# Kernel optimization log

Hardware: AMD Instinct MI355X
Metric: run time of the kernel (lower is better)

## Reference

```python
import jax, jax.numpy as jnp
import numpy as np

EPS = 1e-6
HEAD_DIM = 64
N_Q = 16
N_KV = 2

def setup_inputs() -> dict:
    key = jax.random.key(0)
    ks = jax.random.split(key, 4)
    H = 1024
    x = jax.random.normal(ks[0], (4, 8192, H), dtype=jnp.float32)
    ln_weight = jnp.zeros((H,), dtype=jnp.float32)  # Gemma param; scale is (1 + w)
    wq = jax.random.normal(ks[1], (H, HEAD_DIM * N_Q), dtype=jnp.float32) / np.sqrt(H)
    wk = jax.random.normal(ks[2], (H, HEAD_DIM * N_KV), dtype=jnp.float32) / np.sqrt(H)
    wv = jax.random.normal(ks[3], (H, HEAD_DIM * N_KV), dtype=jnp.float32) / np.sqrt(H)
    return {"x": x, "ln_weight": ln_weight, "wq": wq, "wk": wk, "wv": wv}

def gemma_rms_norm(x, w):
    xf = x.astype(jnp.float32)
    h = xf * jax.lax.rsqrt(jnp.mean(xf * xf, axis=-1, keepdims=True) + EPS)
    return (h * (1.0 + w.astype(jnp.float32))).astype(x.dtype)

def reference(x, ln_weight, wq, wk, wv):
    # Gemma RMSNorm prologue, then three linear projections (no bias).
    h = gemma_rms_norm(x, ln_weight)            # [B, S, H]
    q = jnp.einsum('bsh,hd->bsd', h, wq)        # [B, S, nq*d]
    k = jnp.einsum('bsh,hd->bsd', h, wk)        # [B, S, nkv*d]
    v = jnp.einsum('bsh,hd->bsd', h, wv)
    B, S = x.shape[0], x.shape[1]
    q = q.reshape(B, S, N_Q, HEAD_DIM)
    k = k.reshape(B, S, N_KV, HEAD_DIM)
    v = v.reshape(B, S, N_KV, HEAD_DIM)
    return (q, k, v)
```

## Files before the change

kernel.cpp:

```cpp
#include <hip/hip_runtime.h>
#include <hip/hip_bf16.h>

typedef __attribute__((ext_vector_type(4))) float f32x4;
typedef __attribute__((ext_vector_type(8))) short bf16x8;

#define H 1024
#define NTOT 1280
#define BM 256
#define BN 256
#define BK 64
#define NKT (H / BK)

static __device__ __forceinline__ unsigned short f2bf(float f) {
    __hip_bfloat16 b = __float2bfloat16(f);
    return __builtin_bit_cast(unsigned short, b);
}

#define GLOAD_LDS16(g, l)                                                     \
    __builtin_amdgcn_global_load_lds(                                         \
        (const __attribute__((address_space(1))) void*)(g),                   \
        (__attribute__((address_space(3))) void*)(l), 16, 0, 0)

__global__ __launch_bounds__(256) void k_rms(const float* __restrict__ x,
                                             __hip_bfloat16* __restrict__ h) {
    const int wave = threadIdx.x >> 6;
    const int lane = threadIdx.x & 63;
    const size_t row = (size_t)blockIdx.x * 4 + wave;

    const float4* xr = (const float4*)(x + row * H);
    float4 v[4];
    float ss = 0.f;
#pragma unroll
    for (int i = 0; i < 4; ++i) {
        v[i] = xr[lane + 64 * i];
        ss += v[i].x * v[i].x + v[i].y * v[i].y + v[i].z * v[i].z + v[i].w * v[i].w;
    }
#pragma unroll
    for (int o = 1; o < 64; o <<= 1) ss += __shfl_xor(ss, o);
    const float sc = rsqrtf(ss * (1.0f / H) + 1e-6f);

    ushort4* hr = (ushort4*)(h + row * H);
#pragma unroll
    for (int i = 0; i < 4; ++i) {
        ushort4 o4;
        o4.x = f2bf(v[i].x * sc);
        o4.y = f2bf(v[i].y * sc);
        o4.z = f2bf(v[i].z * sc);
        o4.w = f2bf(v[i].w * sc);
        hr[lane + 64 * i] = o4;
    }
}

__global__ __launch_bounds__(256) void k_wprep(const float* __restrict__ wq,
                                               const float* __restrict__ wk,
                                               const float* __restrict__ wv,
                                               const float* __restrict__ lnw,
                                               __hip_bfloat16* __restrict__ Bt) {
    const int idx = blockIdx.x * 256 + threadIdx.x;
    const int n = idx >> 10;
    const int k = idx & 1023;
    const float s = 1.0f + lnw[k];
    float w;
    if (n < 1024)       w = wq[k * 1024 + n];
    else if (n < 1152)  w = wk[k * 128 + (n - 1024)];
    else                w = wv[k * 128 + (n - 1152)];
    Bt[idx] = __float2bfloat16(s * w);
}

__global__ __launch_bounds__(512, 2) void k_gemm(const __hip_bfloat16* __restrict__ A,
                                                 const __hip_bfloat16* __restrict__ Bt,
                                                 float* __restrict__ out, int rows) {
    __shared__ __align__(16) char smem[131072];

    const int tid = threadIdx.x;
    const int lane = tid & 63;
    const int wid = tid >> 6;
    const int wm = wid >> 2;
    const int wn = wid & 3;

    const int nwg = gridDim.x;
    const int q8 = nwg >> 3, r8 = nwg & 7;
    const int xcd = blockIdx.x & 7, rank = blockIdx.x >> 3;
    const int wg = (xcd < r8 ? xcd * (q8 + 1) : r8 * (q8 + 1) + (xcd - r8) * q8) + rank;
    const int nt = wg % (NTOT / BN);
    const int mt = wg / (NTOT / BN);
    const size_t m0 = (size_t)mt * BM;

    const int cswz = ((tid & 7) * 16) ^ (((tid >> 3) & 7) << 4);
    const char* aG = (const char*)A + (m0 + (tid >> 3)) * (size_t)(H * 2) + cswz;
    const char* bG = (const char*)Bt + ((size_t)nt * BN + (tid >> 3)) * (size_t)(H * 2) + cswz;

#define STAGE(buf, kt)                                                        \
    {                                                                         \
        const char* as_ = aG + (size_t)(kt) * (BK * 2);                       \
        const char* bs_ = bG + (size_t)(kt) * (BK * 2);                       \
        char* ld_ = smem + (buf) * 65536 + tid * 16;                          \
        _Pragma("unroll") for (int j = 0; j < 4; ++j)                         \
            GLOAD_LDS16(as_ + (size_t)j * 64 * (H * 2), ld_ + j * 8192);      \
        _Pragma("unroll") for (int j = 0; j < 4; ++j)                         \
            GLOAD_LDS16(bs_ + (size_t)j * 64 * (H * 2), ld_ + 32768 + j * 8192); \
    }

    const int rowA = wm * 128 + (lane & 15);
    const int rowB = wn * 64 + (lane & 15);
    const int xm = (lane & 7) << 4;
    const int c0 = (((lane >> 4) * 16)) ^ xm;
    const int c1 = (64 + ((lane >> 4) * 16)) ^ xm;

    f32x4 acc[8][4] = {};

    STAGE(0, 0);
    STAGE(1, 1);

#define ITER(kt, DOSTAGE, VMSTR)                                              \
    {                                                                         \
        const int cur_ = (kt) & 1;                                            \
        const char* aLb = smem + cur_ * 65536;                                \
        const char* bLb = aLb + 32768;                                        \
        asm volatile("s_waitcnt vmcnt(" VMSTR ")" ::: "memory");              \
        __builtin_amdgcn_s_barrier();                                         \
        __builtin_amdgcn_sched_barrier(0);                                    \
        bf16x8 a0[8], b0[4];                                                  \
        _Pragma("unroll") for (int mi = 0; mi < 8; ++mi)                      \
            a0[mi] = *(const bf16x8*)(aLb + (rowA + mi * 16) * 128 + c0);     \
        _Pragma("unroll") for (int ni = 0; ni < 4; ++ni)                      \
            b0[ni] = *(const bf16x8*)(bLb + (rowB + ni * 16) * 128 + c0);     \
        _Pragma("unroll") for (int mi = 0; mi < 8; ++mi)                      \
            _Pragma("unroll") for (int ni = 0; ni < 4; ++ni)                  \
                acc[mi][ni] = __builtin_amdgcn_mfma_f32_16x16x32_bf16(        \
                    a0[mi], b0[ni], acc[mi][ni], 0, 0, 0);                    \
        bf16x8 a1[8], b1[4];                                                  \
        _Pragma("unroll") for (int mi = 0; mi < 8; ++mi)                      \
            a1[mi] = *(const bf16x8*)(aLb + (rowA + mi * 16) * 128 + c1);     \
        _Pragma("unroll") for (int ni = 0; ni < 4; ++ni)                      \
            b1[ni] = *(const bf16x8*)(bLb + (rowB + ni * 16) * 128 + c1);     \
        asm volatile("s_waitcnt lgkmcnt(0)" ::: "memory");                    \
        __builtin_amdgcn_s_barrier();                                         \
        __builtin_amdgcn_sched_barrier(0);                                    \
        if (DOSTAGE) STAGE(cur_, (kt) + 2);                                   \
        _Pragma("unroll") for (int mi = 0; mi < 8; ++mi)                      \
            _Pragma("unroll") for (int ni = 0; ni < 4; ++ni)                  \
                acc[mi][ni] = __builtin_amdgcn_mfma_f32_16x16x32_bf16(        \
                    a1[mi], b1[ni], acc[mi][ni], 0, 0, 0);                    \
    }

#pragma unroll 2
    for (int kt = 0; kt < NKT - 2; ++kt) ITER(kt, true, "8");
    ITER(NKT - 2, false, "8");
    ITER(NKT - 1, false, "0");

    const size_t QSZ = (size_t)rows * 1024;
    const size_t KSZ = (size_t)rows * 128;
    const int colg0 = nt * BN + wn * 64;
    float* op;
    int ldc, cb0;
    if (colg0 < 1024)      { op = out;             ldc = 1024; cb0 = colg0; }
    else if (colg0 < 1152) { op = out + QSZ;       ldc = 128;  cb0 = colg0 - 1024; }
    else                   { op = out + QSZ + KSZ; ldc = 128;  cb0 = colg0 - 1152; }

    const size_t r0 = m0 + wm * 128 + ((lane >> 4) * 4);
    const int cc0 = cb0 + (lane & 15);
#pragma unroll
    for (int mi = 0; mi < 8; ++mi)
#pragma unroll
        for (int ni = 0; ni < 4; ++ni)
#pragma unroll
            for (int r = 0; r < 4; ++r)
                op[(r0 + mi * 16 + r) * (size_t)ldc + cc0 + ni * 16] = acc[mi][ni][r];
}

extern "C" void kernel_launch(void* const* d_in, const int* in_sizes, int n_in,
                              void* d_out, int out_size, void* d_ws, size_t ws_size,
                              hipStream_t stream) {
    const float* x   = (const float*)d_in[0];
    const float* lnw = (const float*)d_in[1];
    const float* wq  = (const float*)d_in[2];
    const float* wk  = (const float*)d_in[3];
    const float* wv  = (const float*)d_in[4];
    float* out = (float*)d_out;

    const int rows = in_sizes[0] / H;

    __hip_bfloat16* Bt = (__hip_bfloat16*)d_ws;
    __hip_bfloat16* h  = (__hip_bfloat16*)((char*)d_ws + (size_t)NTOT * H * 2);

    k_wprep<<<NTOT * H / 256, 256, 0, stream>>>(wq, wk, wv, lnw, Bt);
    k_rms<<<rows / 4, 256, 0, stream>>>(x, h);
    k_gemm<<<(rows / BM) * (NTOT / BN), 512, 0, stream>>>(h, Bt, out, rows);
}
```

Measured before the change: 155.5 us.

## Split GEMM k-tile into four barrier-separated MFMA phases with setprio

```diff
diff --git a/kernel.cpp b/kernel.cpp
--- a/kernel.cpp
+++ b/kernel.cpp
@@ -112,42 +112,67 @@
     STAGE(0, 0);
     STAGE(1, 1);
 
-#define ITER(kt, DOSTAGE, VMSTR)                                              \
+#define MFMA4x4(AF, BF, MIOFF)                                                \
+    _Pragma("unroll") for (int mi = 0; mi < 4; ++mi)                          \
+        _Pragma("unroll") for (int ni = 0; ni < 4; ++ni)                      \
+            acc[(MIOFF) + mi][ni] = __builtin_amdgcn_mfma_f32_16x16x32_bf16(  \
+                AF[mi], BF[ni], acc[(MIOFF) + mi][ni], 0, 0, 0);
+
+#define TILE(cur, kt, DOSTAGE, VMSTR)                                         \
     {                                                                         \
-        const int cur_ = (kt) & 1;                                            \
-        const char* aLb = smem + cur_ * 65536;                                \
+        const char* aLb = smem + (cur) * 65536;                               \
         const char* bLb = aLb + 32768;                                        \
+                                                                      \
         asm volatile("s_waitcnt vmcnt(" VMSTR ")" ::: "memory");              \
         __builtin_amdgcn_s_barrier();                                         \
-        __builtin_amdgcn_sched_barrier(0);                                    \
-        bf16x8 a0[8], b0[4];                                                  \
-        _Pragma("unroll") for (int mi = 0; mi < 8; ++mi)                      \
-            a0[mi] = *(const bf16x8*)(aLb + (rowA + mi * 16) * 128 + c0);     \
+        bf16x8 a0h0[4], b0[4];                                                \
+        _Pragma("unroll") for (int mi = 0; mi < 4; ++mi)                      \
+            a0h0[mi] = *(const bf16x8*)(aLb + (rowA + mi * 16) * 128 + c0);   \
         _Pragma("unroll") for (int ni = 0; ni < 4; ++ni)                      \
             b0[ni] = *(const bf16x8*)(bLb + (rowB + ni * 16) * 128 + c0);     \
-        _Pragma("unroll") for (int mi = 0; mi < 8; ++mi)                      \
-            _Pragma("unroll") for (int ni = 0; ni < 4; ++ni)                  \
-                acc[mi][ni] = __builtin_amdgcn_mfma_f32_16x16x32_bf16(        \
-                    a0[mi], b0[ni], acc[mi][ni], 0, 0, 0);                    \
-        bf16x8 a1[8], b1[4];                                                  \
-        _Pragma("unroll") for (int mi = 0; mi < 8; ++mi)                      \
-            a1[mi] = *(const bf16x8*)(aLb + (rowA + mi * 16) * 128 + c1);     \
+        __builtin_amdgcn_s_barrier();                                         \
+        asm volatile("s_waitcnt lgkmcnt(0)" ::: "memory");                    \
+        __builtin_amdgcn_s_setprio(1);                                        \
+        MFMA4x4(a0h0, b0, 0);                                                 \
+        __builtin_amdgcn_s_setprio(0);                                        \
+                                                                      \
+        bf16x8 a0h1[4];                                                       \
+        _Pragma("unroll") for (int mi = 0; mi < 4; ++mi)                      \
+            a0h1[mi] = *(const bf16x8*)(aLb + (rowA + 64 + mi * 16) * 128 + c0); \
+        __builtin_amdgcn_s_barrier();                                         \
+        asm volatile("s_waitcnt lgkmcnt(0)" ::: "memory");                    \
+        __builtin_amdgcn_s_setprio(1);                                        \
+        MFMA4x4(a0h1, b0, 4);                                                 \
+        __builtin_amdgcn_s_setprio(0);                                        \
+                                                                      \
+        bf16x8 a1h0[4], b1[4];                                                \
+        _Pragma("unroll") for (int mi = 0; mi < 4; ++mi)                      \
+            a1h0[mi] = *(const bf16x8*)(aLb + (rowA + mi * 16) * 128 + c1);   \
         _Pragma("unroll") for (int ni = 0; ni < 4; ++ni)                      \
             b1[ni] = *(const bf16x8*)(bLb + (rowB + ni * 16) * 128 + c1);     \
-        asm volatile("s_waitcnt lgkmcnt(0)" ::: "memory");                    \
-        __builtin_amdgcn_s_barrier();                                         \
-        __builtin_amdgcn_sched_barrier(0);                                    \
-        if (DOSTAGE) STAGE(cur_, (kt) + 2);                                   \
-        _Pragma("unroll") for (int mi = 0; mi < 8; ++mi)                      \
-            _Pragma("unroll") for (int ni = 0; ni < 4; ++ni)                  \
-                acc[mi][ni] = __builtin_amdgcn_mfma_f32_16x16x32_bf16(        \
-                    a1[mi], b1[ni], acc[mi][ni], 0, 0, 0);                    \
-    }
-
-#pragma unroll 2
-    for (int kt = 0; kt < NKT - 2; ++kt) ITER(kt, true, "8");
-    ITER(NKT - 2, false, "8");
-    ITER(NKT - 1, false, "0");
+        __builtin_amdgcn_s_barrier();                                         \
+        asm volatile("s_waitcnt lgkmcnt(0)" ::: "memory");                    \
+        __builtin_amdgcn_s_setprio(1);                                        \
+        MFMA4x4(a1h0, b1, 0);                                                 \
+        __builtin_amdgcn_s_setprio(0);                                        \
+                                                                      \
+        bf16x8 a1h1[4];                                                       \
+        _Pragma("unroll") for (int mi = 0; mi < 4; ++mi)                      \
+            a1h1[mi] = *(const bf16x8*)(aLb + (rowA + 64 + mi * 16) * 128 + c1); \
+        asm volatile("s_waitcnt lgkmcnt(0)" ::: "memory");                    \
+        __builtin_amdgcn_s_barrier();                                         \
+        if (DOSTAGE) STAGE(cur, (kt) + 2);                                    \
+        __builtin_amdgcn_s_setprio(1);                                        \
+        MFMA4x4(a1h1, b1, 4);                                                 \
+        __builtin_amdgcn_s_setprio(0);                                        \
+    }
+
+    for (int kt = 0; kt < NKT - 2; kt += 2) {
+        TILE(0, kt, true, "8");
+        TILE(1, kt + 1, true, "8");
+    }
+    TILE(0, NKT - 2, false, "8");
+    TILE(1, NKT - 1, false, "0");
 
     const size_t QSZ = (size_t)rows * 1024;
     const size_t KSZ = (size_t)rows * 128;
```

After: 156.6 us. Within noise of the previous version (+0.7%).

## Fuse RMSNorm into GEMM by loading fp32 x and scaling rows in epilogue

Applied to the files above, without the earlier changes.

```diff
diff --git a/kernel.cpp b/kernel.cpp
--- a/kernel.cpp
+++ b/kernel.cpp
@@ -9,7 +9,7 @@
 #define BM 256
 #define BN 256
 #define BK 64
-#define NKT (H / BK)
+#define NKT 16
 
 static __device__ __forceinline__ unsigned short f2bf(float f) {
     __hip_bfloat16 b = __float2bfloat16(f);
@@ -20,36 +20,6 @@
     __builtin_amdgcn_global_load_lds(                                         \
         (const __attribute__((address_space(1))) void*)(g),                   \
         (__attribute__((address_space(3))) void*)(l), 16, 0, 0)
-
-__global__ __launch_bounds__(256) void k_rms(const float* __restrict__ x,
-                                             __hip_bfloat16* __restrict__ h) {
-    const int wave = threadIdx.x >> 6;
-    const int lane = threadIdx.x & 63;
-    const size_t row = (size_t)blockIdx.x * 4 + wave;
-
-    const float4* xr = (const float4*)(x + row * H);
-    float4 v[4];
-    float ss = 0.f;
-#pragma unroll
-    for (int i = 0; i < 4; ++i) {
-        v[i] = xr[lane + 64 * i];
-        ss += v[i].x * v[i].x + v[i].y * v[i].y + v[i].z * v[i].z + v[i].w * v[i].w;
-    }
-#pragma unroll
-    for (int o = 1; o < 64; o <<= 1) ss += __shfl_xor(ss, o);
-    const float sc = rsqrtf(ss * (1.0f / H) + 1e-6f);
-
-    ushort4* hr = (ushort4*)(h + row * H);
-#pragma unroll
-    for (int i = 0; i < 4; ++i) {
-        ushort4 o4;
-        o4.x = f2bf(v[i].x * sc);
-        o4.y = f2bf(v[i].y * sc);
-        o4.z = f2bf(v[i].z * sc);
-        o4.w = f2bf(v[i].w * sc);
-        hr[lane + 64 * i] = o4;
-    }
-}
 
 __global__ __launch_bounds__(256) void k_wprep(const float* __restrict__ wq,
                                                const float* __restrict__ wk,
@@ -67,10 +37,11 @@
     Bt[idx] = __float2bfloat16(s * w);
 }
 
-__global__ __launch_bounds__(512, 2) void k_gemm(const __hip_bfloat16* __restrict__ A,
+__global__ __launch_bounds__(512, 2) void k_gemm(const float* __restrict__ X,
                                                  const __hip_bfloat16* __restrict__ Bt,
                                                  float* __restrict__ out, int rows) {
     __shared__ __align__(16) char smem[131072];
+    __shared__ float s_lds[BM];
 
     const int tid = threadIdx.x;
     const int lane = tid & 63;
@@ -86,20 +57,37 @@
     const int mt = wg / (NTOT / BN);
     const size_t m0 = (size_t)mt * BM;
 
-    const int cswz = ((tid & 7) * 16) ^ (((tid >> 3) & 7) << 4);
-    const char* aG = (const char*)A + (m0 + (tid >> 3)) * (size_t)(H * 2) + cswz;
-    const char* bG = (const char*)Bt + ((size_t)nt * BN + (tid >> 3)) * (size_t)(H * 2) + cswz;
-
-#define STAGE(buf, kt)                                                        \
-    {                                                                         \
-        const char* as_ = aG + (size_t)(kt) * (BK * 2);                       \
-        const char* bs_ = bG + (size_t)(kt) * (BK * 2);                       \
-        char* ld_ = smem + (buf) * 65536 + tid * 16;                          \
-        _Pragma("unroll") for (int j = 0; j < 4; ++j)                         \
-            GLOAD_LDS16(as_ + (size_t)j * 64 * (H * 2), ld_ + j * 8192);      \
-        _Pragma("unroll") for (int j = 0; j < 4; ++j)                         \
-            GLOAD_LDS16(bs_ + (size_t)j * 64 * (H * 2), ld_ + 32768 + j * 8192); \
-    }
+    const int rq = tid >> 3;
+    const int c8 = (tid & 7) * 8;
+    const float* xbase = X + (m0 + rq) * (size_t)H + c8;
+    const int adst = rq * 128 + (((tid & 7) * 16) ^ ((rq & 7) << 4));
+    const int cswz = ((tid & 7) * 16) ^ ((rq & 7) << 4);
+    const char* bG = (const char*)Bt + ((size_t)nt * BN + rq) * (size_t)(H * 2) + cswz;
+
+    float4 va[8];
+    float ss[4] = {0.f, 0.f, 0.f, 0.f};
+
+#define A_ISSUE(kt)                                                           \
+    _Pragma("unroll") for (int q = 0; q < 4; ++q) {                           \
+        va[q * 2]     = *(const float4*)(xbase + (size_t)(kt) * 64 + (size_t)q * 64 * H); \
+        va[q * 2 + 1] = *(const float4*)(xbase + (size_t)(kt) * 64 + (size_t)q * 64 * H + 4); \
+    }
+
+#define A_CVTWRITE(buf)                                                       \
+    _Pragma("unroll") for (int q = 0; q < 4; ++q) {                           \
+        float4 f0 = va[q * 2], f1 = va[q * 2 + 1];                            \
+        ss[q] += f0.x * f0.x + f0.y * f0.y + f0.z * f0.z + f0.w * f0.w;       \
+        ss[q] += f1.x * f1.x + f1.y * f1.y + f1.z * f1.z + f1.w * f1.w;       \
+        bf16x8 pk;                                                            \
+        pk[0] = f2bf(f0.x); pk[1] = f2bf(f0.y); pk[2] = f2bf(f0.z); pk[3] = f2bf(f0.w); \
+        pk[4] = f2bf(f1.x); pk[5] = f2bf(f1.y); pk[6] = f2bf(f1.z); pk[7] = f2bf(f1.w); \
+        *(bf16x8*)(smem + (size_t)(buf) * 65536 + adst + q * 8192) = pk;      \
+    }
+
+#define STAGE_B(buf, kt)                                                      \
+    _Pragma("unroll") for (int q = 0; q < 4; ++q)                             \
+        GLOAD_LDS16(bG + (size_t)(kt) * (BK * 2) + (size_t)q * 64 * (H * 2),  \
+                    smem + (buf) * 65536 + 32768 + q * 8192 + tid * 16);
 
     const int rowA = wm * 128 + (lane & 15);
     const int rowB = wn * 64 + (lane & 15);
@@ -109,45 +97,66 @@
 
     f32x4 acc[8][4] = {};
 
-    STAGE(0, 0);
-    STAGE(1, 1);
-
-#define ITER(kt, DOSTAGE, VMSTR)                                              \
+#define COMPUTE(cur)                                                          \
     {                                                                         \
-        const int cur_ = (kt) & 1;                                            \
-        const char* aLb = smem + cur_ * 65536;                                \
-        const char* bLb = aLb + 32768;                                        \
-        asm volatile("s_waitcnt vmcnt(" VMSTR ")" ::: "memory");              \
+        const char* aL = smem + (cur) * 65536;                                \
+        const char* bL = aL + 32768;                                          \
+        bf16x8 b0[4];                                                         \
+        _Pragma("unroll") for (int ni = 0; ni < 4; ++ni)                      \
+            b0[ni] = *(const bf16x8*)(bL + (rowB + ni * 16) * 128 + c0);      \
+        _Pragma("unroll") for (int mi = 0; mi < 8; ++mi) {                    \
+            bf16x8 a = *(const bf16x8*)(aL + (rowA + mi * 16) * 128 + c0);    \
+            _Pragma("unroll") for (int ni = 0; ni < 4; ++ni)                  \
+                acc[mi][ni] = __builtin_amdgcn_mfma_f32_16x16x32_bf16(        \
+                    a, b0[ni], acc[mi][ni], 0, 0, 0);                         \
+        }                                                                     \
+        bf16x8 b1[4];                                                         \
+        _Pragma("unroll") for (int ni = 0; ni < 4; ++ni)                      \
+            b1[ni] = *(const bf16x8*)(bL + (rowB + ni * 16) * 128 + c1);      \
+        _Pragma("unroll") for (int mi = 0; mi < 8; ++mi) {                    \
+            bf16x8 a = *(const bf16x8*)(aL + (rowA + mi * 16) * 128 + c1);    \
+            _Pragma("unroll") for (int ni = 0; ni < 4; ++ni)                  \
+                acc[mi][ni] = __builtin_amdgcn_mfma_f32_16x16x32_bf16(        \
+                    a, b1[ni], acc[mi][ni], 0, 0, 0);                         \
+        }                                                                     \
+    }
+
+#define TILE(cur, kt, DS, VM)                                                 \
+    {                                                                         \
+        if (DS) A_ISSUE((kt) + 2);                                            \
+        COMPUTE(cur);                                                         \
+        asm volatile("s_waitcnt vmcnt(" VM ") lgkmcnt(0)" ::: "memory");      \
+        __builtin_amdgcn_sched_barrier(0);                                    \
         __builtin_amdgcn_s_barrier();                                         \
         __builtin_amdgcn_sched_barrier(0);                                    \
-        bf16x8 a0[8], b0[4];                                                  \
-        _Pragma("unroll") for (int mi = 0; mi < 8; ++mi)                      \
-            a0[mi] = *(const bf16x8*)(aLb + (rowA + mi * 16) * 128 + c0);     \
-        _Pragma("unroll") for (int ni = 0; ni < 4; ++ni)                      \
-            b0[ni] = *(const bf16x8*)(bLb + (rowB + ni * 16) * 128 + c0);     \
-        _Pragma("unroll") for (int mi = 0; mi < 8; ++mi)                      \
-            _Pragma("unroll") for (int ni = 0; ni < 4; ++ni)                  \
-                acc[mi][ni] = __builtin_amdgcn_mfma_f32_16x16x32_bf16(        \
-                    a0[mi], b0[ni], acc[mi][ni], 0, 0, 0);                    \
-        bf16x8 a1[8], b1[4];                                                  \
-        _Pragma("unroll") for (int mi = 0; mi < 8; ++mi)                      \
-            a1[mi] = *(const bf16x8*)(aLb + (rowA + mi * 16) * 128 + c1);     \
-        _Pragma("unroll") for (int ni = 0; ni < 4; ++ni)                      \
-            b1[ni] = *(const bf16x8*)(bLb + (rowB + ni * 16) * 128 + c1);     \
-        asm volatile("s_waitcnt lgkmcnt(0)" ::: "memory");                    \
-        __builtin_amdgcn_s_barrier();                                         \
-        __builtin_amdgcn_sched_barrier(0);                                    \
-        if (DOSTAGE) STAGE(cur_, (kt) + 2);                                   \
-        _Pragma("unroll") for (int mi = 0; mi < 8; ++mi)                      \
-            _Pragma("unroll") for (int ni = 0; ni < 4; ++ni)                  \
-                acc[mi][ni] = __builtin_amdgcn_mfma_f32_16x16x32_bf16(        \
-                    a1[mi], b1[ni], acc[mi][ni], 0, 0, 0);                    \
-    }
-
-#pragma unroll 2
-    for (int kt = 0; kt < NKT - 2; ++kt) ITER(kt, true, "8");
-    ITER(NKT - 2, false, "8");
-    ITER(NKT - 1, false, "0");
+        if (DS) { STAGE_B(cur, (kt) + 2); A_CVTWRITE(cur); }                  \
+    }
+
+    A_ISSUE(0); STAGE_B(0, 0);
+    A_CVTWRITE(0);
+    A_ISSUE(1); STAGE_B(1, 1);
+    A_CVTWRITE(1);
+    asm volatile("s_waitcnt lgkmcnt(0)" ::: "memory");
+    __builtin_amdgcn_sched_barrier(0);
+    __builtin_amdgcn_s_barrier();
+    __builtin_amdgcn_sched_barrier(0);
+
+    for (int kt = 0; kt < NKT - 2; kt += 2) {
+        TILE(0, kt, 1, "8");
+        TILE(1, kt + 1, 1, "8");
+    }
+    TILE(0, NKT - 2, 0, "0");
+    TILE(1, NKT - 1, 0, "0");
+
+#pragma unroll
+    for (int q = 0; q < 4; ++q) {
+        float s = ss[q];
+        s += __shfl_xor(s, 1);
+        s += __shfl_xor(s, 2);
+        s += __shfl_xor(s, 4);
+        s_lds[(tid >> 3) + q * 64] = rsqrtf(s * (1.0f / H) + 1e-6f);
+    }
+    __syncthreads();
 
     const size_t QSZ = (size_t)rows * 1024;
     const size_t KSZ = (size_t)rows * 128;
@@ -158,15 +167,19 @@
     else if (colg0 < 1152) { op = out + QSZ;       ldc = 128;  cb0 = colg0 - 1024; }
     else                   { op = out + QSZ + KSZ; ldc = 128;  cb0 = colg0 - 1152; }
 
-    const size_t r0 = m0 + wm * 128 + ((lane >> 4) * 4);
+    const int rl0 = wm * 128 + ((lane >> 4) * 4);
+    const size_t r0 = m0 + rl0;
     const int cc0 = cb0 + (lane & 15);
 #pragma unroll
     for (int mi = 0; mi < 8; ++mi)
 #pragma unroll
-        for (int ni = 0; ni < 4; ++ni)
-#pragma unroll
-            for (int r = 0; r < 4; ++r)
-                op[(r0 + mi * 16 + r) * (size_t)ldc + cc0 + ni * 16] = acc[mi][ni][r];
+        for (int r = 0; r < 4; ++r) {
+            const float sc = s_lds[rl0 + mi * 16 + r];
+#pragma unroll
+            for (int ni = 0; ni < 4; ++ni)
+                op[(r0 + mi * 16 + r) * (size_t)ldc + cc0 + ni * 16] =
+                    acc[mi][ni][r] * sc;
+        }
 }
 
 extern "C" void kernel_launch(void* const* d_in, const int* in_sizes, int n_in,
@@ -182,9 +195,7 @@
     const int rows = in_sizes[0] / H;
 
     __hip_bfloat16* Bt = (__hip_bfloat16*)d_ws;
-    __hip_bfloat16* h  = (__hip_bfloat16*)((char*)d_ws + (size_t)NTOT * H * 2);
 
     k_wprep<<<NTOT * H / 256, 256, 0, stream>>>(wq, wk, wv, lnw, Bt);
-    k_rms<<<rows / 4, 256, 0, stream>>>(x, h);
-    k_gemm<<<(rows / BM) * (NTOT / BN), 512, 0, stream>>>(h, Bt, out, rows);
-}
+    k_gemm<<<(rows / BM) * (NTOT / BN), 512, 0, stream>>>(x, Bt, out, rows);
+}
```

New measurement: 284.0 us. 1.83x slower.

## Shrink GEMM M-tile, split B staging into halves, and transpose weights via LDS

Applied to the files above, without the earlier changes.

```diff
diff --git a/kernel.cpp b/kernel.cpp
--- a/kernel.cpp
+++ b/kernel.cpp
@@ -6,10 +6,11 @@
 
 #define H 1024
 #define NTOT 1280
-#define BM 256
+#define BM 128
 #define BN 256
 #define BK 64
-#define NKT (H / BK)
+#define NKT 16
+#define NTILES 5
 
 static __device__ __forceinline__ unsigned short f2bf(float f) {
     __hip_bfloat16 b = __float2bfloat16(f);
@@ -56,114 +57,156 @@
                                                const float* __restrict__ wv,
                                                const float* __restrict__ lnw,
                                                __hip_bfloat16* __restrict__ Bt) {
-    const int idx = blockIdx.x * 256 + threadIdx.x;
-    const int n = idx >> 10;
-    const int k = idx & 1023;
-    const float s = 1.0f + lnw[k];
-    float w;
-    if (n < 1024)       w = wq[k * 1024 + n];
-    else if (n < 1152)  w = wk[k * 128 + (n - 1024)];
-    else                w = wv[k * 128 + (n - 1152)];
-    Bt[idx] = __float2bfloat16(s * w);
+    __shared__ float l[64][65];
+    const int t = threadIdx.x;
+    const int kt = blockIdx.x & 15;
+    const int ntl = blockIdx.x >> 4;
+    const int k0 = kt * 64, n0 = ntl * 64;
+    const float* src; int ldn, nb;
+    if (n0 < 1024)      { src = wq; ldn = 1024; nb = n0; }
+    else if (n0 < 1152) { src = wk; ldn = 128;  nb = n0 - 1024; }
+    else                { src = wv; ldn = 128;  nb = n0 - 1152; }
+    const int nl = t & 63, kl = t >> 6;
+#pragma unroll
+    for (int i = 0; i < 16; ++i) {
+        const int k = kl + i * 4;
+        l[k][nl] = (1.0f + lnw[k0 + k]) * src[(size_t)(k0 + k) * ldn + nb + nl];
+    }
+    __syncthreads();
+    const int k2 = t & 63, n2 = t >> 6;
+#pragma unroll
+    for (int i = 0; i < 16; ++i) {
+        const int n = n2 + i * 4;
+        Bt[(size_t)(n0 + n) * 1024 + k0 + k2] = __float2bfloat16(l[k2][n]);
+    }
 }
 
 __global__ __launch_bounds__(512, 2) void k_gemm(const __hip_bfloat16* __restrict__ A,
                                                  const __hip_bfloat16* __restrict__ Bt,
                                                  float* __restrict__ out, int rows) {
-    __shared__ __align__(16) char smem[131072];
+    __shared__ __align__(16) char smem[98304];
 
     const int tid = threadIdx.x;
     const int lane = tid & 63;
     const int wid = tid >> 6;
-    const int wm = wid >> 2;
-    const int wn = wid & 3;
-
-    const int nwg = gridDim.x;
-    const int q8 = nwg >> 3, r8 = nwg & 7;
-    const int xcd = blockIdx.x & 7, rank = blockIdx.x >> 3;
-    const int wg = (xcd < r8 ? xcd * (q8 + 1) : r8 * (q8 + 1) + (xcd - r8) * q8) + rank;
-    const int nt = wg % (NTOT / BN);
-    const int mt = wg / (NTOT / BN);
+    const int wm = wid >> 1;
+    const int wn = wid & 1;
+
+    const int cpx = gridDim.x >> 3;
+    const int wg = (blockIdx.x & 7) * cpx + (blockIdx.x >> 3);
+    const int nt = wg % NTILES;
+    const int mt = wg / NTILES;
     const size_t m0 = (size_t)mt * BM;
 
     const int cswz = ((tid & 7) * 16) ^ (((tid >> 3) & 7) << 4);
     const char* aG = (const char*)A + (m0 + (tid >> 3)) * (size_t)(H * 2) + cswz;
     const char* bG = (const char*)Bt + ((size_t)nt * BN + (tid >> 3)) * (size_t)(H * 2) + cswz;
 
-#define STAGE(buf, kt)                                                        \
-    {                                                                         \
-        const char* as_ = aG + (size_t)(kt) * (BK * 2);                       \
-        const char* bs_ = bG + (size_t)(kt) * (BK * 2);                       \
-        char* ld_ = smem + (buf) * 65536 + tid * 16;                          \
-        _Pragma("unroll") for (int j = 0; j < 4; ++j)                         \
-            GLOAD_LDS16(as_ + (size_t)j * 64 * (H * 2), ld_ + j * 8192);      \
-        _Pragma("unroll") for (int j = 0; j < 4; ++j)                         \
-            GLOAD_LDS16(bs_ + (size_t)j * 64 * (H * 2), ld_ + 32768 + j * 8192); \
-    }
-
-    const int rowA = wm * 128 + (lane & 15);
-    const int rowB = wn * 64 + (lane & 15);
+#define STAGE_A2(buf, kt)                                                     \
+    { GLOAD_LDS16(aG + (size_t)(kt) * 128,                                    \
+                  smem + (buf) * 49152 + tid * 16);                           \
+      GLOAD_LDS16(aG + (size_t)(kt) * 128 + (size_t)64 * (H * 2),             \
+                  smem + (buf) * 49152 + 8192 + tid * 16); }
+#define STAGE_B02(buf, kt)                                                    \
+    { GLOAD_LDS16(bG + (size_t)(kt) * 128,                                    \
+                  smem + (buf) * 49152 + 16384 + tid * 16);                   \
+      GLOAD_LDS16(bG + (size_t)(kt) * 128 + (size_t)128 * (H * 2),            \
+                  smem + (buf) * 49152 + 16384 + 16384 + tid * 16); }
+#define STAGE_B13(buf, kt)                                                    \
+    { GLOAD_LDS16(bG + (size_t)(kt) * 128 + (size_t)64 * (H * 2),             \
+                  smem + (buf) * 49152 + 16384 + 8192 + tid * 16);            \
+      GLOAD_LDS16(bG + (size_t)(kt) * 128 + (size_t)192 * (H * 2),            \
+                  smem + (buf) * 49152 + 16384 + 24576 + tid * 16); }
+
+    const int rowA = wm * 32 + (lane & 15);
+    const int rowB = wn * 128 + (lane & 15);
     const int xm = (lane & 7) << 4;
     const int c0 = (((lane >> 4) * 16)) ^ xm;
     const int c1 = (64 + ((lane >> 4) * 16)) ^ xm;
 
-    f32x4 acc[8][4] = {};
-
-    STAGE(0, 0);
-    STAGE(1, 1);
-
-#define ITER(kt, DOSTAGE, VMSTR)                                              \
+    f32x4 acc[2][8] = {};
+
+#define MFMAP(AK0, AK1, B0, B1, NIOFF)                                        \
+    _Pragma("unroll") for (int mi = 0; mi < 2; ++mi)                          \
+        _Pragma("unroll") for (int ni = 0; ni < 4; ++ni)                      \
+            acc[mi][(NIOFF) + ni] = __builtin_amdgcn_mfma_f32_16x16x32_bf16(  \
+                AK0[mi], B0[ni], acc[mi][(NIOFF) + ni], 0, 0, 0);             \
+    _Pragma("unroll") for (int mi = 0; mi < 2; ++mi)                          \
+        _Pragma("unroll") for (int ni = 0; ni < 4; ++ni)                      \
+            acc[mi][(NIOFF) + ni] = __builtin_amdgcn_mfma_f32_16x16x32_bf16(  \
+                AK1[mi], B1[ni], acc[mi][(NIOFF) + ni], 0, 0, 0);
+
+#define TILE(cur, kt, CARRY, DS, VM)                                          \
     {                                                                         \
-        const int cur_ = (kt) & 1;                                            \
-        const char* aLb = smem + cur_ * 65536;                                \
-        const char* bLb = aLb + 32768;                                        \
-        asm volatile("s_waitcnt vmcnt(" VMSTR ")" ::: "memory");              \
-        __builtin_amdgcn_s_barrier();                                         \
+        const char* aL = smem + (cur) * 49152;                                \
+        const char* bL = aL + 16384;                                          \
+                                                            \
+        if (CARRY) STAGE_B13((cur) ^ 1, (kt) + 1);                            \
+        bf16x8 ak0[2], ak1[2], b0k0[4], b0k1[4];                              \
+        _Pragma("unroll") for (int mi = 0; mi < 2; ++mi) {                    \
+            ak0[mi] = *(const bf16x8*)(aL + (rowA + mi * 16) * 128 + c0);     \
+            ak1[mi] = *(const bf16x8*)(aL + (rowA + mi * 16) * 128 + c1);     \
+        }                                                                     \
+        _Pragma("unroll") for (int ni = 0; ni < 4; ++ni) {                    \
+            b0k0[ni] = *(const bf16x8*)(bL + (rowB + ni * 16) * 128 + c0);    \
+            b0k1[ni] = *(const bf16x8*)(bL + (rowB + ni * 16) * 128 + c1);    \
+        }                                                                     \
+        asm volatile("s_waitcnt lgkmcnt(8)" ::: "memory");                    \
+        __builtin_amdgcn_s_barrier();                                         \
+        asm volatile("s_waitcnt lgkmcnt(0)" ::: "memory");                    \
+        __builtin_amdgcn_s_setprio(1);                                        \
+        MFMAP(ak0, ak1, b0k0, b0k1, 0);                                       \
+        __builtin_amdgcn_s_setprio(0);                                        \
+        __builtin_amdgcn_s_barrier();                                         \
+                                                            \
+        if (DS) { STAGE_A2(cur, (kt) + 2); STAGE_B02(cur, (kt) + 2); }        \
+        bf16x8 b1k0[4], b1k1[4];                                              \
+        _Pragma("unroll") for (int ni = 0; ni < 4; ++ni) {                    \
+            b1k0[ni] = *(const bf16x8*)(bL + (rowB + 64 + ni * 16) * 128 + c0); \
+            b1k1[ni] = *(const bf16x8*)(bL + (rowB + 64 + ni * 16) * 128 + c1); \
+        }                                                                     \
+        __builtin_amdgcn_s_barrier();                                         \
+        asm volatile("s_waitcnt lgkmcnt(0)" ::: "memory");                    \
+        __builtin_amdgcn_s_setprio(1);                                        \
+        MFMAP(ak0, ak1, b1k0, b1k1, 4);                                       \
+        __builtin_amdgcn_s_setprio(0);                                        \
+        asm volatile("s_waitcnt vmcnt(" VM ")" ::: "memory");                 \
         __builtin_amdgcn_sched_barrier(0);                                    \
-        bf16x8 a0[8], b0[4];                                                  \
-        _Pragma("unroll") for (int mi = 0; mi < 8; ++mi)                      \
-            a0[mi] = *(const bf16x8*)(aLb + (rowA + mi * 16) * 128 + c0);     \
-        _Pragma("unroll") for (int ni = 0; ni < 4; ++ni)                      \
-            b0[ni] = *(const bf16x8*)(bLb + (rowB + ni * 16) * 128 + c0);     \
-        _Pragma("unroll") for (int mi = 0; mi < 8; ++mi)                      \
-            _Pragma("unroll") for (int ni = 0; ni < 4; ++ni)                  \
-                acc[mi][ni] = __builtin_amdgcn_mfma_f32_16x16x32_bf16(        \
-                    a0[mi], b0[ni], acc[mi][ni], 0, 0, 0);                    \
-        bf16x8 a1[8], b1[4];                                                  \
-        _Pragma("unroll") for (int mi = 0; mi < 8; ++mi)                      \
-            a1[mi] = *(const bf16x8*)(aLb + (rowA + mi * 16) * 128 + c1);     \
-        _Pragma("unroll") for (int ni = 0; ni < 4; ++ni)                      \
-            b1[ni] = *(const bf16x8*)(bLb + (rowB + ni * 16) * 128 + c1);     \
-        asm volatile("s_waitcnt lgkmcnt(0)" ::: "memory");                    \
         __builtin_amdgcn_s_barrier();                                         \
         __builtin_amdgcn_sched_barrier(0);                                    \
-        if (DOSTAGE) STAGE(cur_, (kt) + 2);                                   \
-        _Pragma("unroll") for (int mi = 0; mi < 8; ++mi)                      \
-            _Pragma("unroll") for (int ni = 0; ni < 4; ++ni)                  \
-                acc[mi][ni] = __builtin_amdgcn_mfma_f32_16x16x32_bf16(        \
-                    a1[mi], b1[ni], acc[mi][ni], 0, 0, 0);                    \
-    }
-
-#pragma unroll 2
-    for (int kt = 0; kt < NKT - 2; ++kt) ITER(kt, true, "8");
-    ITER(NKT - 2, false, "8");
-    ITER(NKT - 1, false, "0");
+    }
+
+    STAGE_A2(0, 0); STAGE_B02(0, 0); STAGE_B13(0, 0);
+    STAGE_A2(1, 1); STAGE_B02(1, 1); STAGE_B13(1, 1);
+    asm volatile("s_waitcnt vmcnt(6)" ::: "memory");
+    __builtin_amdgcn_sched_barrier(0);
+    __builtin_amdgcn_s_barrier();
+    __builtin_amdgcn_sched_barrier(0);
+
+    TILE(0, 0, 0, 1, "4");
+    TILE(1, 1, 1, 1, "4");
+    for (int kt = 2; kt <= 12; kt += 2) {
+        TILE(0, kt, 1, 1, "4");
+        TILE(1, kt + 1, 1, 1, "4");
+    }
+    TILE(0, 14, 1, 0, "0");
+    TILE(1, 15, 0, 0, "0");
 
     const size_t QSZ = (size_t)rows * 1024;
     const size_t KSZ = (size_t)rows * 128;
-    const int colg0 = nt * BN + wn * 64;
+    const int colg0 = nt * BN + wn * 128;
     float* op;
     int ldc, cb0;
     if (colg0 < 1024)      { op = out;             ldc = 1024; cb0 = colg0; }
     else if (colg0 < 1152) { op = out + QSZ;       ldc = 128;  cb0 = colg0 - 1024; }
     else                   { op = out + QSZ + KSZ; ldc = 128;  cb0 = colg0 - 1152; }
 
-    const size_t r0 = m0 + wm * 128 + ((lane >> 4) * 4);
+    const size_t r0 = m0 + wm * 32 + ((lane >> 4) * 4);
     const int cc0 = cb0 + (lane & 15);
 #pragma unroll
-    for (int mi = 0; mi < 8; ++mi)
-#pragma unroll
-        for (int ni = 0; ni < 4; ++ni)
+    for (int mi = 0; mi < 2; ++mi)
+#pragma unroll
+        for (int ni = 0; ni < 8; ++ni)
 #pragma unroll
             for (int r = 0; r < 4; ++r)
                 op[(r0 + mi * 16 + r) * (size_t)ldc + cc0 + ni * 16] = acc[mi][ni][r];
@@ -184,7 +227,7 @@
     __hip_bfloat16* Bt = (__hip_bfloat16*)d_ws;
     __hip_bfloat16* h  = (__hip_bfloat16*)((char*)d_ws + (size_t)NTOT * H * 2);
 
-    k_wprep<<<NTOT * H / 256, 256, 0, stream>>>(wq, wk, wv, lnw, Bt);
+    k_wprep<<<320, 256, 0, stream>>>(wq, wk, wv, lnw, Bt);
     k_rms<<<rows / 4, 256, 0, stream>>>(x, h);
-    k_gemm<<<(rows / BM) * (NTOT / BN), 512, 0, stream>>>(h, Bt, out, rows);
-}
+    k_gemm<<<(rows / BM) * NTILES, 512, 0, stream>>>(h, Bt, out, rows);
+}
```

Measured after the change: 151.7 us. 1.02x faster.
